# Kernel tuning notes

Measured on AMD Instinct MI355X. Metric: run time of the kernel, lower is better.

## Reference

```python
import jax, jax.numpy as jnp
import numpy as np

B, TGT, SRC, DIM = 8, 1024, 1024, 1024

def setup_inputs() -> dict:
    key = jax.random.key(0)
    k1, k2, k3, k4, k5 = jax.random.split(key, 5)
    s = 1.0 / np.sqrt(DIM)
    return {
        "input": jax.random.normal(k1, (B, TGT, DIM), dtype=jnp.float32),
        "context": jax.random.normal(k2, (B, SRC, DIM), dtype=jnp.float32),
        "context_lengths": jax.random.randint(k3, (B,), 1, SRC + 1, dtype=jnp.int64 if jax.config.jax_enable_x64 else jnp.int32),
        "W_in": jax.random.normal(k4, (DIM, DIM), dtype=jnp.float32) * s,   # torch Linear weight [out,in]
        "W_out": jax.random.normal(k5, (DIM, 2 * DIM), dtype=jnp.float32) * s,
    }

def reference(input, context, context_lengths, W_in, W_out):
    # GlobalAttention, attn_type='general', include_rnn=True, dropout=0 (identity)
    # score: (W_in @ h_t) . h_s  -> [B, TGT, SRC]
    h_t = jnp.einsum('btd,ed->bte', input, W_in)
    align = jnp.einsum('bte,bse->bts', h_t, context)
    # mask positions >= length with -inf before softmax over source dim
    mask = jnp.arange(align.shape[-1])[None, :] < context_lengths[:, None]  # [B, SRC]
    align = jnp.where(mask[:, None, :], align, -jnp.inf)
    align_vectors = jax.nn.softmax(align, axis=-1)                         # [B, TGT, SRC]
    c = jnp.einsum('bts,bsd->btd', align_vectors, context)                 # context vector
    concat = jnp.concatenate([c, input], axis=-1)                          # [B, TGT, 2*DIM]
    attn_h = jnp.tanh(jnp.einsum('btf,df->btd', concat, W_out))            # linear_out (no bias) + tanh
    return attn_h, align_vectors
```

## Files before the change

kernel.cpp:

```cpp
#include <hip/hip_runtime.h>

typedef __attribute__((ext_vector_type(8))) short short8;
typedef __attribute__((ext_vector_type(4))) float f32x4;

#define DIM  1024
#define BT   8192
#define NBAT 8
#define KSOFF (1 << 29)

__device__ __forceinline__ unsigned short f2bf(float x){
  union { float f; unsigned u; } un; un.f = x;
  unsigned r = un.u + 0x7fffu + ((un.u >> 16) & 1u);
  return (unsigned short)(r >> 16);
}
__device__ __forceinline__ float bf2f(unsigned short h){
  union { unsigned u; float f; } un; un.u = ((unsigned)h) << 16;
  return un.f;
}

__global__ void prep_kernel(const float* __restrict__ in,
                            unsigned short* __restrict__ in_hi,
                            unsigned short* __restrict__ in_lo,
                            const float* __restrict__ Win,
                            unsigned short* __restrict__ wi_hi,
                            unsigned short* __restrict__ wi_lo,
                            const float* __restrict__ Wout,
                            unsigned short* __restrict__ wo_hi){
  const int N0 = (BT * DIM) >> 2;
  const int N1 = N0 + ((DIM * DIM) >> 2);
  const int N2 = N1 + ((DIM * 2 * DIM) >> 2);
  int stride = gridDim.x * blockDim.x;
  for (int i = blockIdx.x * blockDim.x + threadIdx.x; i < N2; i += stride){
    if (i < N0){
      float4 v = ((const float4*)in)[i];
      ushort4 h, l;
      h.x = f2bf(v.x); l.x = f2bf(v.x - bf2f(h.x));
      h.y = f2bf(v.y); l.y = f2bf(v.y - bf2f(h.y));
      h.z = f2bf(v.z); l.z = f2bf(v.z - bf2f(h.z));
      h.w = f2bf(v.w); l.w = f2bf(v.w - bf2f(h.w));
      ((ushort4*)in_hi)[i] = h;
      ((ushort4*)in_lo)[i] = l;
    } else if (i < N1){
      int j = i - N0;
      float4 v = ((const float4*)Win)[j];
      ushort4 h, l;
      h.x = f2bf(v.x); l.x = f2bf(v.x - bf2f(h.x));
      h.y = f2bf(v.y); l.y = f2bf(v.y - bf2f(h.y));
      h.z = f2bf(v.z); l.z = f2bf(v.z - bf2f(h.z));
      h.w = f2bf(v.w); l.w = f2bf(v.w - bf2f(h.w));
      ((ushort4*)wi_hi)[j] = h;
      ((ushort4*)wi_lo)[j] = l;
    } else {
      int j = i - N1;
      float4 v = ((const float4*)Wout)[j];
      ushort4 h;
      h.x = f2bf(v.x); h.y = f2bf(v.y); h.z = f2bf(v.z); h.w = f2bf(v.w);
      ((ushort4*)wo_hi)[j] = h;
    }
  }
}

__global__ void ctx_prep_kernel(const float* __restrict__ ctx,
                                unsigned short* __restrict__ hi,
                                unsigned short* __restrict__ lo,
                                unsigned short* __restrict__ ctxT){
  __shared__ unsigned short t[64][65];
  int bz = blockIdx.z;
  int s0 = blockIdx.x << 6, d0 = blockIdx.y << 6;
  int tx = threadIdx.x, ty = threadIdx.y;
  const size_t base = (((size_t)bz << 10) + s0) * DIM + d0;
  const float* src = ctx + base;
  unsigned short* hrow = hi + base;
  unsigned short* lrow = lo + base;
  #pragma unroll
  for (int i = ty; i < 64; i += 4){
    float v = src[(size_t)i * DIM + tx];
    unsigned short h = f2bf(v);
    hrow[(size_t)i * DIM + tx] = h;
    lrow[(size_t)i * DIM + tx] = f2bf(v - bf2f(h));
    t[i][tx] = h;
  }
  __syncthreads();
  unsigned short* dst = ctxT + (((size_t)bz << 10) + d0) * DIM + s0;
  #pragma unroll
  for (int i = ty; i < 64; i += 4)
    dst[(size_t)i * DIM + tx] = t[tx][i];
}

__global__ __launch_bounds__(256) void softmax_kernel(float* __restrict__ sc,
                                                      unsigned short* __restrict__ Pb,
                                                      const int* __restrict__ lens){
  const int row = blockIdx.x;
  const int len = lens[row >> 10];
  const int tid = threadIdx.x;
  const int lane = tid & 63, wid = tid >> 6;
  float* rp = sc + ((size_t)row << 10);
  const int s0 = tid << 2;
  float4 v;
  if (s0 < len) v = ((const float4*)rp)[tid];
  else          v = (float4){0.f, 0.f, 0.f, 0.f};
  float x0 = (s0 + 0 < len) ? v.x : -INFINITY;
  float x1 = (s0 + 1 < len) ? v.y : -INFINITY;
  float x2 = (s0 + 2 < len) ? v.z : -INFINITY;
  float x3 = (s0 + 3 < len) ? v.w : -INFINITY;
  float wmax = fmaxf(fmaxf(x0, x1), fmaxf(x2, x3));
  #pragma unroll
  for (int o = 32; o > 0; o >>= 1) wmax = fmaxf(wmax, __shfl_xor(wmax, o));
  __shared__ float red[8];
  if (lane == 0) red[wid] = wmax;
  __syncthreads();
  float mx = fmaxf(fmaxf(red[0], red[1]), fmaxf(red[2], red[3]));
  float e0 = (s0 + 0 < len) ? __expf(x0 - mx) : 0.f;
  float e1 = (s0 + 1 < len) ? __expf(x1 - mx) : 0.f;
  float e2 = (s0 + 2 < len) ? __expf(x2 - mx) : 0.f;
  float e3 = (s0 + 3 < len) ? __expf(x3 - mx) : 0.f;
  float ws = e0 + e1 + e2 + e3;
  #pragma unroll
  for (int o = 32; o > 0; o >>= 1) ws += __shfl_xor(ws, o);
  if (lane == 0) red[4 + wid] = ws;
  __syncthreads();
  float inv = 1.f / (red[4] + red[5] + red[6] + red[7]);
  float4 p; p.x = e0 * inv; p.y = e1 * inv; p.z = e2 * inv; p.w = e3 * inv;
  ((float4*)rp)[tid] = p;
  ushort4 pb; pb.x = f2bf(p.x); pb.y = f2bf(p.y); pb.z = f2bf(p.z); pb.w = f2bf(p.w);
  ((ushort4*)(Pb + ((size_t)row << 10)))[tid] = pb;
}

__device__ __forceinline__ int lds_off(int r, int kb){
  return r * 64 + (((kb ^ ((r >> 1) & 3))) << 4);
}

__device__ __forceinline__ void gld16(void* lds, const void* g){
  __builtin_amdgcn_global_load_lds(
      (__attribute__((address_space(1))) void*)(g),
      (__attribute__((address_space(3))) void*)(lds), 16, 0, 0);
}

template<bool SPLIT, int EPI, int KSPLIT>
__global__ __launch_bounds__(256, 2) void gemm_kernel(
    const unsigned short* __restrict__ Ah,  const unsigned short* __restrict__ Al,
    const unsigned short* __restrict__ Ah2, const unsigned short* __restrict__ Al2,
    const unsigned short* __restrict__ Bh,  const unsigned short* __restrict__ Bl,
    int K, int lda, int ldb,
    long long aStride, long long bStride, long long oStride,
    float* __restrict__ outF, unsigned short* __restrict__ o1,
    unsigned short* __restrict__ o2, int ldo,
    const int* __restrict__ lens, int lmode)
{
  constexpr int TILE = 128 * 64;
  __shared__ __align__(16) char smem[(SPLIT ? 4 : 2) * TILE];
  char* sAh = smem;
  char* sBh = smem + TILE;
  char* sAl = smem + (SPLIT ? 2 : 0) * TILE;
  char* sBl = smem + (SPLIT ? 3 : 0) * TILE;

  const int tid  = threadIdx.x;
  const int lane = tid & 63;
  const int wid  = tid >> 6;
  const int z    = blockIdx.z;

  int bx = blockIdx.x, by = blockIdx.y;
  if (gridDim.x == 8 && gridDim.y == 8){
    int o = bx + (by << 3);
    int k = o & 7, j = o >> 3;
    bx = ((k & 3) << 1) | (j & 1);  by = ((k >> 2) << 2) | (j >> 1);
  } else if (gridDim.x == 8 && (gridDim.y & 7) == 0){
    int o = bx + (by << 3);
    int xcd = o & 7, j = o >> 3;
    bx = j & 7;
    by = xcd * (gridDim.y >> 3) + (j >> 3);
  }
  const int m0 = by * 128;
  const int n0 = bx * 128;

  int Keff = K;
  if (lmode){
    const int len = lens[z];
    if (lmode == 1 && n0 >= len) return;
    if (lmode == 2){
      int kc = (len + 31) & ~31;
      Keff = kc < K ? kc : K;
    }
  }

  const unsigned short* gAh  = Ah  + (size_t)z * aStride + (size_t)m0 * lda;
  const unsigned short* gAh2 = Ah2 + (size_t)z * aStride + (size_t)m0 * lda;
  const unsigned short* gBh  = Bh  + (size_t)z * bStride + (size_t)n0 * ldb;
  const unsigned short* gAl  = SPLIT ? (Al  + (size_t)z * aStride + (size_t)m0 * lda) : (const unsigned short*)0;
  const unsigned short* gAl2 = SPLIT ? (Al2 + (size_t)z * aStride + (size_t)m0 * lda) : (const unsigned short*)0;
  const unsigned short* gBl  = SPLIT ? (Bl  + (size_t)z * bStride + (size_t)n0 * ldb) : (const unsigned short*)0;

  const int rS0 = (wid << 5) + (lane >> 2);
  const int rS1 = rS0 + 16;
  const int cS0 = ((lane & 3) ^ ((rS0 >> 1) & 3)) << 3;
  const int cS1 = ((lane & 3) ^ ((rS1 >> 1) & 3)) << 3;
  const int dS0 = (wid << 5) << 6;
  const int dS1 = dS0 + (16 << 6);
  const unsigned short* qAh0  = gAh  + (size_t)rS0 * lda + cS0;
  const unsigned short* qAh1  = gAh  + (size_t)rS1 * lda + cS1;
  const unsigned short* qAh20 = gAh2 + (size_t)rS0 * lda + cS0;
  const unsigned short* qAh21 = gAh2 + (size_t)rS1 * lda + cS1;
  const unsigned short* qBh0  = gBh  + (size_t)rS0 * ldb + cS0;
  const unsigned short* qBh1  = gBh  + (size_t)rS1 * ldb + cS1;
  const unsigned short* qAl0  = SPLIT ? (gAl  + (size_t)rS0 * lda + cS0) : (const unsigned short*)0;
  const unsigned short* qAl1  = SPLIT ? (gAl  + (size_t)rS1 * lda + cS1) : (const unsigned short*)0;
  const unsigned short* qAl20 = SPLIT ? (gAl2 + (size_t)rS0 * lda + cS0) : (const unsigned short*)0;
  const unsigned short* qAl21 = SPLIT ? (gAl2 + (size_t)rS1 * lda + cS1) : (const unsigned short*)0;
  const unsigned short* qBl0  = SPLIT ? (gBl  + (size_t)rS0 * ldb + cS0) : (const unsigned short*)0;
  const unsigned short* qBl1  = SPLIT ? (gBl  + (size_t)rS1 * ldb + cS1) : (const unsigned short*)0;

  f32x4 acc[4][4];
  #pragma unroll
  for (int m = 0; m < 4; m++)
    #pragma unroll
    for (int n = 0; n < 4; n++)
      acc[m][n] = (f32x4){0.f, 0.f, 0.f, 0.f};

  const int wr = (wid >> 1) * 64;
  const int wc = (wid & 1) * 64;
  const int fr = lane & 15;
  const int kb = lane >> 4;

  for (int k0 = 0; k0 < Keff; k0 += 32){
    __syncthreads();
    const unsigned short *a0, *a1, *l0 = 0, *l1 = 0;
    if (KSPLIT != KSOFF && k0 >= KSPLIT){
      int q = k0 - KSPLIT;
      a0 = qAh20 + q; a1 = qAh21 + q;
      if (SPLIT){ l0 = qAl20 + q; l1 = qAl21 + q; }
    } else {
      a0 = qAh0 + k0; a1 = qAh1 + k0;
      if (SPLIT){ l0 = qAl0 + k0; l1 = qAl1 + k0; }
    }
    gld16(sAh + dS0, a0);
    gld16(sAh + dS1, a1);
    gld16(sBh + dS0, qBh0 + k0);
    gld16(sBh + dS1, qBh1 + k0);
    if (SPLIT){
      gld16(sAl + dS0, l0);
      gld16(sAl + dS1, l1);
      gld16(sBl + dS0, qBl0 + k0);
      gld16(sBl + dS1, qBl1 + k0);
    }
    __syncthreads();

    short8 ah[4], bh[4], al[4], bl[4];
    #pragma unroll
    for (int m = 0; m < 4; m++){
      int off = lds_off(wr + m * 16 + fr, kb);
      ah[m] = *(const short8*)(sAh + off);
      if (SPLIT) al[m] = *(const short8*)(sAl + off);
    }
    #pragma unroll
    for (int n = 0; n < 4; n++){
      int off = lds_off(wc + n * 16 + fr, kb);
      bh[n] = *(const short8*)(sBh + off);
      if (SPLIT) bl[n] = *(const short8*)(sBl + off);
    }
    #pragma unroll
    for (int m = 0; m < 4; m++)
      #pragma unroll
      for (int n = 0; n < 4; n++){
        acc[m][n] = __builtin_amdgcn_mfma_f32_16x16x32_bf16(ah[m], bh[n], acc[m][n], 0, 0, 0);
        if (SPLIT){
          acc[m][n] = __builtin_amdgcn_mfma_f32_16x16x32_bf16(ah[m], bl[n], acc[m][n], 0, 0, 0);
          acc[m][n] = __builtin_amdgcn_mfma_f32_16x16x32_bf16(al[m], bh[n], acc[m][n], 0, 0, 0);
        }
      }
  }

  const int rbase = (lane >> 4) * 2 * 2;
  const int cbase = lane & 15;
  #pragma unroll
  for (int m = 0; m < 4; m++){
    #pragma unroll
    for (int n = 0; n < 4; n++){
      f32x4 v = acc[m][n];
      int col = n0 + wc + n * 16 + cbase;
      #pragma unroll
      for (int j = 0; j < 4; j++){
        int row = m0 + wr + m * 16 + rbase + j;
        float val = v[j];
        size_t idx = (size_t)row * ldo + col;
        if (EPI == 0){
          unsigned short h = f2bf(val);
          o1[(size_t)z * oStride + idx] = h;
          o2[(size_t)z * oStride + idx] = f2bf(val - bf2f(h));
        } else if (EPI == 1){
          outF[(size_t)z * oStride + idx] = val;
        } else if (EPI == 4){
          o1[(size_t)z * oStride + idx] = f2bf(val);
        } else {
          outF[idx] = tanhf(val);
        }
      }
    }
  }
}

extern "C" void kernel_launch(void* const* d_in, const int* in_sizes, int n_in,
                              void* d_out, int out_size, void* d_ws, size_t ws_size,
                              hipStream_t stream){
  const float* input   = (const float*)d_in[0];
  const float* context = (const float*)d_in[1];
  const int*   lens    = (const int*)d_in[2];
  const float* Win     = (const float*)d_in[3];
  const float* Wout    = (const float*)d_in[4];
  float* attn  = (float*)d_out;
  float* align = attn + (size_t)BT * DIM;

  char* ws = (char*)d_ws;
  size_t off = 0;
  auto alloc = [&](size_t bytes) -> char* {
    char* p = ws + off; off += (bytes + 255) & ~(size_t)255; return p;
  };
  const size_t MTD = (size_t)BT * DIM;
  unsigned short* in_hi = (unsigned short*)alloc(MTD * 2);
  unsigned short* in_lo = (unsigned short*)alloc(MTD * 2);
  unsigned short* cx_hi = (unsigned short*)alloc(MTD * 2);
  unsigned short* cx_lo = (unsigned short*)alloc(MTD * 2);
  unsigned short* wi_hi = (unsigned short*)alloc((size_t)DIM * DIM * 2);
  unsigned short* wi_lo = (unsigned short*)alloc((size_t)DIM * DIM * 2);
  unsigned short* ht_hi = (unsigned short*)alloc(MTD * 2);
  unsigned short* ht_lo = (unsigned short*)alloc(MTD * 2);
  unsigned short* cxT   = (unsigned short*)alloc(MTD * 2);
  unsigned short* c_hi  = (unsigned short*)alloc(MTD * 2);
  unsigned short* wo_hi = (unsigned short*)alloc((size_t)DIM * 2 * DIM * 2);
  unsigned short* p_bf  = cx_hi;
  if (off > ws_size) return;

  prep_kernel<<<4096, 256, 0, stream>>>(input, in_hi, in_lo,
                                        Win, wi_hi, wi_lo, Wout, wo_hi);
  ctx_prep_kernel<<<dim3(16, 16, NBAT), dim3(64, 4), 0, stream>>>(context, cx_hi, cx_lo, cxT);

  gemm_kernel<true, 0, KSOFF><<<dim3(8, 64, 1), 256, 0, stream>>>(
      in_hi, in_lo, in_hi, in_lo, wi_hi, wi_lo, DIM, DIM, DIM,
      0, 0, 0,
      nullptr, ht_hi, ht_lo, DIM, nullptr, 0);
  gemm_kernel<true, 1, KSOFF><<<dim3(8, 8, NBAT), 256, 0, stream>>>(
      ht_hi, ht_lo, ht_hi, ht_lo, cx_hi, cx_lo, DIM, DIM, DIM,
      (long long)DIM * 1024, (long long)DIM * 1024, (long long)DIM * 1024,
      align, nullptr, nullptr, DIM, lens, 1);
  softmax_kernel<<<BT, 256, 0, stream>>>(align, p_bf, lens);
  gemm_kernel<false, 4, KSOFF><<<dim3(8, 8, NBAT), 256, 0, stream>>>(
      p_bf, nullptr, p_bf, nullptr, cxT, nullptr, DIM, DIM, DIM,
      (long long)DIM * 1024, (long long)DIM * 1024, (long long)1024 * 1024,
      nullptr, c_hi, nullptr, DIM, lens, 2);
  gemm_kernel<false, 3, 1024><<<dim3(8, 64, 1), 256, 0, stream>>>(
      c_hi, nullptr, in_hi, nullptr, wo_hi, nullptr, 2 * DIM, DIM, 2 * DIM,
      0, 0, 0,
      attn, nullptr, nullptr, DIM, nullptr, 0);
}
```

Baseline: 230.1 us.

## Add triple-buffered pipelined GEMM for output projection with XCD-aware tile remap

Replaces the generic GEMM launch for the final linear_out + tanh with a new dedicated kernel. The kernel triple-buffers its shared-memory tiles, issues direct global-to-LDS loads two k-steps ahead, interleaves MFMA groups with barriers and priority hints, and remaps block indices so neighbouring tiles land on the same XCD. The aim is to hide global-load latency and improve L2 locality for the concat-input GEMM. In exchange it adds a specialised code path that depends on fixed sizes and uses more LDS per block, which can lower occupancy.

```diff
diff --git a/kernel.cpp b/kernel.cpp
--- a/kernel.cpp
+++ b/kernel.cpp
@@ -298,6 +298,152 @@
   }
 }
 
+template<int EPI, int NT, int KSPLIT>
+__global__ __launch_bounds__(256, 2) void gemm_pipe128_kernel(
+    const unsigned short* __restrict__ Ah, const unsigned short* __restrict__ Ah2,
+    const unsigned short* __restrict__ Bh,
+    int lda, int ldb,
+    float* __restrict__ outF, unsigned short* __restrict__ o1, int ldo)
+{
+  constexpr int TA  = 8192;
+  constexpr int OFF_B = TA;
+  constexpr int BUF = 2 * TA;
+
+  __shared__ __align__(16) char sm0[BUF];
+  __shared__ __align__(16) char sm1[BUF];
+  __shared__ __align__(16) char sm2[BUF];
+
+  const int tid  = threadIdx.x;
+  const int lane = tid & 63;
+  const int w    = tid >> 6;
+
+  int bx = blockIdx.x, by = blockIdx.y;
+  {
+    int o = bx + (by << 3);
+    int xcd = o & 7, j = o >> 3;
+    bx = j & 7;
+    by = xcd * (gridDim.y >> 3) + (j >> 3);
+  }
+  const int m0 = by << 7;
+  const int n0 = bx << 7;
+
+  const unsigned short* gAh  = Ah  + (size_t)m0 * lda;
+  const unsigned short* gAh2 = Ah2 + (size_t)m0 * lda;
+  const unsigned short* gBh  = Bh  + (size_t)n0 * ldb;
+
+  const int rS0 = (w << 5) + (lane >> 2);
+  const int rS1 = rS0 + 16;
+  const int cS0 = ((lane & 3) ^ ((rS0 >> 1) & 3)) << 3;
+  const int cS1 = ((lane & 3) ^ ((rS1 >> 1) & 3)) << 3;
+  const unsigned short* pA0  = gAh  + (size_t)rS0 * lda + cS0;
+  const unsigned short* pA1  = gAh  + (size_t)rS1 * lda + cS1;
+  const unsigned short* pA20 = gAh2 + (size_t)rS0 * lda + cS0;
+  const unsigned short* pA21 = gAh2 + (size_t)rS1 * lda + cS1;
+  const unsigned short* pB0  = gBh  + (size_t)rS0 * ldb + cS0;
+  const unsigned short* pB1  = gBh  + (size_t)rS1 * ldb + cS1;
+  const int dS0 = (w << 5) << 6;
+  const int dS1 = dS0 + (16 << 6);
+
+  f32x4 acc[4][4];
+  #pragma unroll
+  for (int m = 0; m < 4; m++)
+    #pragma unroll
+    for (int n = 0; n < 4; n++)
+      acc[m][n] = (f32x4){0.f, 0.f, 0.f, 0.f};
+
+  const int wr = (w >> 1) << 6;
+  const int wc = (w & 1) << 6;
+  const int fr = lane & 15;
+  const int kb = lane >> 4;
+
+  short8 ah, bh[4];
+
+#define STAGE(WR, KS) do { int _k = (KS);                                   \
+    const unsigned short *_s0, *_s1;                                        \
+    if (_k >= KSPLIT){ int _q = _k - KSPLIT; _s0 = pA20 + _q; _s1 = pA21 + _q; } \
+    else             { _s0 = pA0 + _k;       _s1 = pA1 + _k; }              \
+    gld16(WR + dS0, _s0);                                                   \
+    gld16(WR + dS1, _s1);                                                   \
+    gld16(WR + OFF_B + dS0, pB0 + _k);                                      \
+    gld16(WR + OFF_B + dS1, pB1 + _k);                                      \
+  } while(0)
+
+#define READS_B(RD) do {                                                    \
+    _Pragma("unroll")                                                       \
+    for (int n = 0; n < 4; n++)                                             \
+      bh[n] = *(const short8*)((RD) + OFF_B + lds_off(wc + n * 16 + fr, kb)); \
+  } while(0)
+
+#define READS_A(RD, M)                                                      \
+    ah = *(const short8*)((RD) + lds_off(wr + (M) * 16 + fr, kb))
+
+#define MFMA_M(M) do {                                                      \
+    __builtin_amdgcn_s_setprio(1);                                          \
+    _Pragma("unroll")                                                       \
+    for (int n = 0; n < 4; n++)                                             \
+      acc[M][n] = __builtin_amdgcn_mfma_f32_16x16x32_bf16(ah, bh[n], acc[M][n], 0, 0, 0); \
+    __builtin_amdgcn_s_setprio(0);                                          \
+  } while(0)
+
+#define BAR() do { __builtin_amdgcn_s_barrier();                            \
+                   asm volatile("" ::: "memory"); } while(0)
+#define LGKM0() asm volatile("s_waitcnt lgkmcnt(0)" ::: "memory")
+#define VMCNT4() asm volatile("s_waitcnt vmcnt(4)" ::: "memory")
+
+#define STEP(RD, WR, T) do {                                                \
+    int _ks = (((T) + 2 < NT) ? (T) + 2 : NT - 1) << 5;   \
+    READS_B(RD); READS_A(RD, 0);                                            \
+    STAGE(WR, _ks);                                                         \
+    BAR(); LGKM0(); MFMA_M(0); BAR();                                       \
+    READS_A(RD, 1);                                                        \
+    BAR(); LGKM0(); MFMA_M(1); BAR();                                       \
+    READS_A(RD, 2);                                                        \
+    BAR(); LGKM0(); MFMA_M(2); BAR();                                       \
+    READS_A(RD, 3);                                                        \
+    BAR(); LGKM0(); MFMA_M(3);                                              \
+    VMCNT4();                                                               \
+    BAR();                                                                  \
+  } while(0)
+
+  STAGE(sm0, 0);
+  STAGE(sm1, 32);
+  VMCNT4();
+  BAR();
+
+  for (int t = 0; t < NT; t += 3){
+    STEP(sm0, sm2, t);
+    if (t + 1 < NT) STEP(sm1, sm0, t + 1);
+    if (t + 2 < NT) STEP(sm2, sm1, t + 2);
+  }
+#undef STAGE
+#undef READS_B
+#undef READS_A
+#undef MFMA_M
+#undef BAR
+#undef LGKM0
+#undef VMCNT4
+#undef STEP
+
+  const int rbase = (lane >> 4) << 2;
+  const int cbase = lane & 15;
+  #pragma unroll
+  for (int m = 0; m < 4; m++){
+    #pragma unroll
+    for (int n = 0; n < 4; n++){
+      f32x4 v = acc[m][n];
+      int col = n0 + wc + n * 16 + cbase;
+      #pragma unroll
+      for (int j = 0; j < 4; j++){
+        int row = m0 + wr + m * 16 + rbase + j;
+        float val = v[j];
+        size_t idx = (size_t)row * ldo + col;
+        if (EPI == 3) outF[idx] = tanhf(val);
+        else          o1[idx] = f2bf(val);
+      }
+    }
+  }
+}
+
 extern "C" void kernel_launch(void* const* d_in, const int* in_sizes, int n_in,
                               void* d_out, int out_size, void* d_ws, size_t ws_size,
                               hipStream_t stream){
@@ -346,8 +492,7 @@
       p_bf, nullptr, p_bf, nullptr, cxT, nullptr, DIM, DIM, DIM,
       (long long)DIM * 1024, (long long)DIM * 1024, (long long)1024 * 1024,
       nullptr, c_hi, nullptr, DIM, lens, 2);
-  gemm_kernel<false, 3, 1024><<<dim3(8, 64, 1), 256, 0, stream>>>(
-      c_hi, nullptr, in_hi, nullptr, wo_hi, nullptr, 2 * DIM, DIM, 2 * DIM,
-      0, 0, 0,
-      attn, nullptr, nullptr, DIM, nullptr, 0);
-}
+  gemm_pipe128_kernel<3, 64, 1024><<<dim3(8, 64), 256, 0, stream>>>(
+      c_hi, in_hi, wo_hi, DIM, 2 * DIM,
+      attn, nullptr, DIM);
+}
```

New measurement: 223.5 us. -2.9%, faster.
